# Performance work log

Hardware: AMD Instinct MI355X
Metric: run time of the kernel (lower is better)

## Reference

```python
import jax, jax.numpy as jnp
import numpy as np

NUM_HEADS = 16
HIDDEN = 1024
B, S = 2, 2048


def setup_inputs() -> dict:
    key = jax.random.key(0)
    ks = jax.random.split(key, 14)
    D = HIDDEN
    scale = 1.0 / np.sqrt(D)
    inp = {
        "query": jax.random.normal(ks[0], (B, S, D), jnp.float32),
        "key_in": jax.random.normal(ks[1], (B, S, D), jnp.float32),
        "value": jax.random.normal(ks[2], (B, S, D), jnp.float32),
        "group_prob": jax.random.uniform(ks[3], (B, S, S), jnp.float32),
        "mask": jax.random.randint(ks[4], (B, S, S), 0, 2, jnp.int32),
        "wq_k": jax.random.normal(ks[5], (D, D), jnp.float32) * scale,
        "wq_b": jnp.zeros((D,), jnp.float32),
        "wk_k": jax.random.normal(ks[6], (D, D), jnp.float32) * scale,
        "wk_b": jnp.zeros((D,), jnp.float32),
        "wv_k": jax.random.normal(ks[7], (D, D), jnp.float32) * scale,
        "wv_b": jnp.zeros((D,), jnp.float32),
        "wo_k": jax.random.normal(ks[8], (D, D), jnp.float32) * scale,
        "wo_b": jnp.zeros((D,), jnp.float32),
    }
    return inp


def _split_heads(x, H):
    b, s, d = x.shape
    return x.reshape(b, s, H, d // H).transpose(0, 2, 1, 3)  # (B,H,S,dh)


def reference(query, key_in, value, group_prob, mask,
              wq_k, wq_b, wk_k, wk_b, wv_k, wv_b, wo_k, wo_b):
    H = NUM_HEADS
    dh = query.shape[-1] // H
    q = _split_heads(query @ wq_k + wq_b, H)
    k = _split_heads(key_in @ wk_k + wk_b, H)
    v = _split_heads(value @ wv_k + wv_b, H)
    # scaled dot-product logits (B,H,Sq,Sk)
    logits = jnp.einsum('bhqd,bhkd->bhqk', q, k) / jnp.sqrt(jnp.asarray(dh, q.dtype))
    neg = (1.0 - mask.astype(q.dtype)) * -1e9
    logits = logits + neg[:, None, :, :]
    attn = jax.nn.softmax(logits, axis=-1)
    # Tree Transformer modulation: post-softmax elementwise scale by group_prob
    attn = attn * group_prob[:, None, :, :]
    out = jnp.einsum('bhqk,bhkd->bhqd', attn, v)
    out = out.transpose(0, 2, 1, 3).reshape(query.shape[0], -1, H * dh)
    return out @ wo_k + wo_b
```

## Files before the change

kernel.cpp:

```cpp
#include <hip/hip_runtime.h>
#include <hip/hip_bf16.h>
#include <stdint.h>

#define B_ 2
#define S_ 2048
#define D_ 1024
#define H_ 16
#define DH 64

typedef __attribute__((ext_vector_type(4))) float f32x4;
typedef __attribute__((ext_vector_type(8))) short s16x8;
typedef __attribute__((ext_vector_type(4))) short s16x4;

__device__ inline short f2bf(float f) {
  union { float f; unsigned u; } v; v.f = f;
  unsigned r = (v.u + 0x7fffu + ((v.u >> 16) & 1u)) >> 16;
  return (short)r;
}

__device__ inline float bfbits_lo(unsigned u) {
  union { unsigned x; float f; } v; v.x = u << 16; return v.f;
}
__device__ inline float bfbits_hi(unsigned u) {
  union { unsigned x; float f; } v; v.x = u & 0xffff0000u; return v.f;
}

__device__ inline float exp2v(float x) {
  float r; asm("v_exp_f32 %0, %1" : "=v"(r) : "v"(x)); return r;
}
__device__ inline unsigned cvtpk(float a, float b) {
  unsigned r; asm("v_cvt_pk_bf16_f32 %0, %1, %2" : "=v"(r) : "v"(a), "v"(b));
  return r;
}

__global__ __launch_bounds__(256) void cvt3_f32_bf16(const float* __restrict__ a,
                                                     const float* __restrict__ b,
                                                     const float* __restrict__ c,
                                                     short* oa, short* ob, short* oc,
                                                     int n) {
  int z = blockIdx.y;
  const float* in = z == 0 ? a : (z == 1 ? b : c);
  short* out = z == 0 ? oa : (z == 1 ? ob : oc);
  int i = (blockIdx.x * 256 + threadIdx.x) * 4;
  if (i < n) {
    float4 v = *(const float4*)(in + i);
    s16x4 o;
    o.x = f2bf(v.x); o.y = f2bf(v.y); o.z = f2bf(v.z); o.w = f2bf(v.w);
    *(s16x4*)(out + i) = o;
  }
}

__global__ __launch_bounds__(256) void transpose_cvt4(
    const float* __restrict__ i0, const float* __restrict__ i1,
    const float* __restrict__ i2, const float* __restrict__ i3,
    short* o0, short* o1, short* o2, short* o3) {
  int z = blockIdx.z;
  const float* in = z == 0 ? i0 : (z == 1 ? i1 : (z == 2 ? i2 : i3));
  short* out = z == 0 ? o0 : (z == 1 ? o1 : (z == 2 ? o2 : o3));
  __shared__ float tile[32][33];
  int bx = blockIdx.x, by = blockIdx.y;
  int x = bx * 32 + threadIdx.x;
#pragma unroll
  for (int i = 0; i < 32; i += 8) {
    int y = by * 32 + threadIdx.y + i;
    tile[threadIdx.y + i][threadIdx.x] = in[(size_t)y * D_ + x];
  }
  __syncthreads();
  int ox = by * 32 + threadIdx.x;
#pragma unroll
  for (int i = 0; i < 32; i += 8) {
    int oy = bx * 32 + threadIdx.y + i;
    out[(size_t)oy * D_ + ox] = f2bf(tile[threadIdx.x][threadIdx.y + i]);
  }
}

__device__ inline void gload_lds16(const void* g, void* l) {
  __builtin_amdgcn_global_load_lds(
      (const __attribute__((address_space(1))) unsigned*)g,
      (__attribute__((address_space(3))) unsigned*)l, 16, 0, 0);
}

#define BM 128
#define BN 128
#define BK 32

__global__ __launch_bounds__(256) void gemm_bt3(
    const short* __restrict__ A0, const short* __restrict__ A1, const short* __restrict__ A2,
    const short* __restrict__ Bt0, const short* __restrict__ Bt1, const short* __restrict__ Bt2,
    const float* __restrict__ bs0, const float* __restrict__ bs1, const float* __restrict__ bs2,
    void* C0, void* C1, void* C2,
    short* __restrict__ vtout, int vtmode,
    const int* __restrict__ mask, const float* __restrict__ gp,
    short* __restrict__ mgpout, int nmg,
    int M, int N, int K, int f32out, float os0, float os1, float os2) {
  int z = blockIdx.y;
  if (z == 3) {
    int i = (blockIdx.x * 256 + threadIdx.x) * 4;
    int stride = gridDim.x * 256 * 4;
    for (; i < nmg; i += stride) {
      int4 m = *(const int4*)(mask + i);
      float4 g = *(const float4*)(gp + i);
      short b0 = f2bf(g.x); if (!b0) b0 = (short)0x0080;
      short b1 = f2bf(g.y); if (!b1) b1 = (short)0x0080;
      short b2 = f2bf(g.z); if (!b2) b2 = (short)0x0080;
      short b3 = f2bf(g.w); if (!b3) b3 = (short)0x0080;
      s16x4 o;
      o.x = m.x ? b0 : 0;
      o.y = m.y ? b1 : 0;
      o.z = m.z ? b2 : 0;
      o.w = m.w ? b3 : 0;
      *(s16x4*)(mgpout + i) = o;
    }
    return;
  }
  const short* A = z == 0 ? A0 : (z == 1 ? A1 : A2);
  const short* Bt = z == 0 ? Bt0 : (z == 1 ? Bt1 : Bt2);
  const float* bias = z == 0 ? bs0 : (z == 1 ? bs1 : bs2);
  void* C = z == 0 ? C0 : (z == 1 ? C1 : C2);
  float oscale = z == 0 ? os0 : (z == 1 ? os1 : os2);

  __shared__ __align__(16) short As[BM * BK];
  __shared__ __align__(16) short Bs[BN * BK];
  int tid = threadIdx.x;
  int lane = tid & 63, wave = tid >> 6;
  int l15 = lane & 15, l4 = lane >> 4;
  int ntn = N / BN;
  int bid = blockIdx.x;
  bid = ((bid & 7) << 5) | (bid >> 3);
  int bm = bid / ntn, bn = bid % ntn;
  int row0 = bm * BM, col0 = bn * BN;
  int wm = (wave >> 1) * 64, wn = (wave & 1) * 64;

  f32x4 acc[4][4] = {};

  for (int k0 = 0; k0 < K; k0 += BK) {
    __syncthreads();
#pragma unroll
    for (int it = 0; it < 2; ++it) {
      int ch = it * 256 + tid;
      int r = ch >> 2, c = (ch & 3) * 8;
      int ldsbase = (it * 256 + wave * 64) * 8;
      gload_lds16(A + (size_t)(row0 + r) * K + k0 + c, &As[ldsbase]);
      gload_lds16(Bt + (size_t)(col0 + r) * K + k0 + c, &Bs[ldsbase]);
    }
    __syncthreads();
    s16x8 af[4], bf[4];
#pragma unroll
    for (int mf = 0; mf < 4; ++mf)
      af[mf] = *(const s16x8*)&As[(wm + mf * 16 + l15) * BK + l4 * 8];
#pragma unroll
    for (int nf = 0; nf < 4; ++nf)
      bf[nf] = *(const s16x8*)&Bs[(wn + nf * 16 + l15) * BK + l4 * 8];
#pragma unroll
    for (int mf = 0; mf < 4; ++mf)
#pragma unroll
      for (int nf = 0; nf < 4; ++nf)
        acc[mf][nf] = __builtin_amdgcn_mfma_f32_16x16x32_bf16(af[mf], bf[nf],
                                                              acc[mf][nf], 0, 0, 0);
  }

  if (vtmode && z == 2) {
    int b = row0 >> 11;
    int h = (col0 + wn) >> 6;
    int sbase = (row0 & (S_ - 1)) + wm + l4 * 4;
    short* vtb = vtout + ((size_t)(b * H_ + h) * DH) * S_;
#pragma unroll
    for (int nf = 0; nf < 4; ++nf) {
      int dh = nf * 16 + l15;
      float bv = bias[col0 + wn + dh];
#pragma unroll
      for (int mf = 0; mf < 4; ++mf) {
        uint2 o;
        o.x = cvtpk(acc[mf][nf][0] + bv, acc[mf][nf][1] + bv);
        o.y = cvtpk(acc[mf][nf][2] + bv, acc[mf][nf][3] + bv);
        *(uint2*)&vtb[(size_t)dh * S_ + sbase + mf * 16] = o;
      }
    }
    return;
  }

#pragma unroll
  for (int nf = 0; nf < 4; ++nf) {
    int gcol = col0 + wn + nf * 16 + l15;
    float bv = bias[gcol];
#pragma unroll
    for (int mf = 0; mf < 4; ++mf) {
#pragma unroll
      for (int r = 0; r < 4; ++r) {
        int grow = row0 + wm + mf * 16 + l4 * 4 + r;
        float v = (acc[mf][nf][r] + bv) * oscale;
        if (f32out)
          ((float*)C)[(size_t)grow * N + gcol] = v;
        else
          ((short*)C)[(size_t)grow * N + gcol] = f2bf(v);
      }
    }
  }
}

#define QB 128
#define NB 64
#define NTILES (S_ / NB)
#define M0_SHIFT 12.0f

__global__ __launch_bounds__(256, 3) void attn_fused(const short* __restrict__ Qp,
                                                     const short* __restrict__ Kp,
                                                     const short* __restrict__ VT,
                                                     const short* __restrict__ MGP,
                                                     short* __restrict__ ctx) {
  __shared__ __align__(16) short Ks[2][64 * 64];
  __shared__ __align__(16) short Vs[2][64 * 64];
  __shared__ __align__(16) short Ps[4][32 * 64];

  int tid = threadIdx.x, lane = tid & 63, wave = tid >> 6;
  int l15 = lane & 15, l4 = lane >> 4;
  int q0 = blockIdx.x * QB;
  int bh = blockIdx.y;
  int b = bh >> 4, h = bh & 15;
  int wq = wave * 32;

  const short* Qbase = Qp + (size_t)b * S_ * D_ + (size_t)h * DH;
  const short* Kbase = Kp + (size_t)b * S_ * D_ + (size_t)h * DH;
  const short* Vbase = VT + (size_t)(b * H_ + h) * DH * S_;
  const short* Mrow0 = MGP + (size_t)b * S_ * S_ + (size_t)(q0 + wq + l15) * S_ + l4 * 4;
  const short* Mrow1 = Mrow0 + (size_t)16 * S_;

  int i0 = tid, i1 = 256 + tid;
  int r0 = i0 >> 3, c0 = (i0 & 7) ^ (r0 & 7);
  int r1 = i1 >> 3, c1 = (i1 & 7) ^ (r1 & 7);
  int ldsA = wave * 512;
  int ldsB = 2048 + wave * 512;

#define STAGE(kv0, buf)                                                       \
  do {                                                                        \
    gload_lds16(Kbase + (size_t)((kv0) + r0) * D_ + c0 * 8, &Ks[buf][ldsA]);  \
    gload_lds16(Kbase + (size_t)((kv0) + r1) * D_ + c1 * 8, &Ks[buf][ldsB]);  \
    gload_lds16(Vbase + (size_t)r0 * S_ + (kv0) + c0 * 8, &Vs[buf][ldsA]);    \
    gload_lds16(Vbase + (size_t)r1 * S_ + (kv0) + c1 * 8, &Vs[buf][ldsB]);    \
  } while (0)

  s16x8 qf[2][2];
#pragma unroll
  for (int mf = 0; mf < 2; ++mf)
#pragma unroll
    for (int ks = 0; ks < 2; ++ks)
      qf[mf][ks] = *(const s16x8*)(Qbase + (size_t)(q0 + wq + mf * 16 + l15) * D_ +
                                   ks * 32 + l4 * 8);

  float lsum[2] = {0.f, 0.f};
  f32x4 oacc[2][4] = {};

  STAGE(0, 0);

  int q7 = l15 & 7;
  short* Pw = &Ps[wave][0];
  int prow[2] = {l15 * 64, (16 + l15) * 64};

  for (int t = 0; t < NTILES; ++t) {
    int buf = t & 1;
    int kvt = t * NB;

    uint2 g2[2][4];
#pragma unroll
    for (int nf = 0; nf < 4; ++nf) {
      g2[0][nf] = *(const uint2*)(Mrow0 + kvt + nf * 16);
      g2[1][nf] = *(const uint2*)(Mrow1 + kvt + nf * 16);
    }
    __builtin_amdgcn_sched_barrier(0);
    if (t + 1 < NTILES) {
      STAGE((t + 1) * NB, buf ^ 1);
      __builtin_amdgcn_sched_barrier(0);
      asm volatile("s_waitcnt vmcnt(12)" ::: "memory");
    } else {
      __builtin_amdgcn_sched_barrier(0);
      asm volatile("s_waitcnt vmcnt(8)" ::: "memory");
    }
    __builtin_amdgcn_s_barrier();
    __builtin_amdgcn_sched_barrier(0);

    f32x4 sacc[2][4] = {};
    __builtin_amdgcn_s_setprio(1);
#pragma unroll
    for (int nf = 0; nf < 4; ++nf) {
      int R = nf * 16 + l15;
#pragma unroll
      for (int ks = 0; ks < 2; ++ks) {
        s16x8 kf = *(const s16x8*)&Ks[buf][R * 64 + (((ks * 4 + l4) ^ q7) * 8)];
#pragma unroll
        for (int mf = 0; mf < 2; ++mf)
          sacc[mf][nf] = __builtin_amdgcn_mfma_f32_16x16x32_bf16(kf, qf[mf][ks],
                                                                 sacc[mf][nf], 0, 0, 0);
      }
    }
    __builtin_amdgcn_s_setprio(0);

    float ee[2][4][4];
#pragma unroll
    for (int mf = 0; mf < 2; ++mf)
#pragma unroll
      for (int nf = 0; nf < 4; ++nf)
#pragma unroll
        for (int r = 0; r < 4; ++r)
          ee[mf][nf][r] = exp2v(sacc[mf][nf][r] - M0_SHIFT);

    if (t + 1 < NTILES)
      asm volatile("s_waitcnt vmcnt(4)" ::: "memory");
    else
      asm volatile("s_waitcnt vmcnt(0)" ::: "memory");
    __builtin_amdgcn_sched_barrier(0);

#pragma unroll
    for (int mf = 0; mf < 2; ++mf) {
#pragma unroll
      for (int nf = 0; nf < 4; ++nf) {
        float gv0 = bfbits_lo(g2[mf][nf].x), gv1 = bfbits_hi(g2[mf][nf].x);
        float gv2 = bfbits_lo(g2[mf][nf].y), gv3 = bfbits_hi(g2[mf][nf].y);
        float e0 = ee[mf][nf][0], e1 = ee[mf][nf][1];
        float e2 = ee[mf][nf][2], e3 = ee[mf][nf][3];
        lsum[mf] += (gv0 != 0.f) ? e0 : 0.f;
        lsum[mf] += (gv1 != 0.f) ? e1 : 0.f;
        lsum[mf] += (gv2 != 0.f) ? e2 : 0.f;
        lsum[mf] += (gv3 != 0.f) ? e3 : 0.f;
        uint2 wp;
        wp.x = cvtpk(e0 * gv0, e1 * gv1);
        wp.y = cvtpk(e2 * gv2, e3 * gv3);
        int gr = ((nf * 2 + (l4 >> 1)) ^ q7) * 8 + (l4 & 1) * 4;
        *(uint2*)&Pw[prow[mf] + gr] = wp;
      }
    }

    __builtin_amdgcn_s_setprio(1);
#pragma unroll
    for (int ks = 0; ks < 2; ++ks) {
      s16x8 pa[2];
#pragma unroll
      for (int mf = 0; mf < 2; ++mf)
        pa[mf] = *(const s16x8*)&Pw[prow[mf] + (((ks * 4 + l4) ^ q7) * 8)];
#pragma unroll
      for (int df = 0; df < 4; ++df) {
        s16x8 vf = *(const s16x8*)&Vs[buf][(df * 16 + l15) * 64 +
                                           (((ks * 4 + l4) ^ q7) * 8)];
#pragma unroll
        for (int mf = 0; mf < 2; ++mf)
          oacc[mf][df] = __builtin_amdgcn_mfma_f32_16x16x32_bf16(vf, pa[mf],
                                                                 oacc[mf][df], 0, 0, 0);
      }
    }
    __builtin_amdgcn_s_setprio(0);

    asm volatile("s_waitcnt lgkmcnt(0)" ::: "memory");
    __builtin_amdgcn_s_barrier();
  }
#undef STAGE

#pragma unroll
  for (int mf = 0; mf < 2; ++mf) {
    float ls = lsum[mf];
    ls += __shfl_xor(ls, 16);
    ls += __shfl_xor(ls, 32);
    float inv = 1.f / ls;
    short* crow = ctx + ((size_t)(b * S_ + q0 + wq + mf * 16 + l15)) * D_ + h * DH;
#pragma unroll
    for (int df = 0; df < 4; ++df) {
      uint2 o;
      o.x = cvtpk(oacc[mf][df][0] * inv, oacc[mf][df][1] * inv);
      o.y = cvtpk(oacc[mf][df][2] * inv, oacc[mf][df][3] * inv);
      *(uint2*)(crow + df * 16 + l4 * 4) = o;
    }
  }
}

extern "C" void kernel_launch(void* const* d_in, const int* in_sizes, int n_in,
                              void* d_out, int out_size, void* d_ws, size_t ws_size,
                              hipStream_t stream) {
  const float* query = (const float*)d_in[0];
  const float* key_in = (const float*)d_in[1];
  const float* value = (const float*)d_in[2];
  const float* group_prob = (const float*)d_in[3];
  const int* mask = (const int*)d_in[4];
  const float* wq_k = (const float*)d_in[5];
  const float* wq_b = (const float*)d_in[6];
  const float* wk_k = (const float*)d_in[7];
  const float* wk_b = (const float*)d_in[8];
  const float* wv_k = (const float*)d_in[9];
  const float* wv_b = (const float*)d_in[10];
  const float* wo_k = (const float*)d_in[11];
  const float* wo_b = (const float*)d_in[12];
  float* out = (float*)d_out;

  short* ws = (short*)d_ws;
  const size_t NT = (size_t)B_ * S_ * D_;
  short* qbf = ws;
  short* kbf = qbf + NT;
  short* vbf = kbf + NT;
  short* wqt = vbf + NT;
  short* wkt = wqt + (size_t)D_ * D_;
  short* wvt = wkt + (size_t)D_ * D_;
  short* wot = wvt + (size_t)D_ * D_;
  short* qp = wot + (size_t)D_ * D_;
  short* kp = qp + NT;
  short* vt = kp + NT;
  short* ctx = vt + NT;
  short* mgp = ws;

  int nblk = (int)(NT / 4 / 256);
  cvt3_f32_bf16<<<dim3(nblk, 3), 256, 0, stream>>>(query, key_in, value,
                                                   qbf, kbf, vbf, (int)NT);

  dim3 tb(32, 8);
  transpose_cvt4<<<dim3(D_ / 32, D_ / 32, 4), tb, 0, stream>>>(
      wq_k, wk_k, wv_k, wo_k, wqt, wkt, wvt, wot);

  int M = B_ * S_;
  int gblocks = (M / BM) * (D_ / BN);
  int nmg = B_ * S_ * S_;
  const float QSCALE = 0.125f * 1.4426950408889634f;
  gemm_bt3<<<dim3(gblocks, 4), 256, 0, stream>>>(
      qbf, kbf, vbf, wqt, wkt, wvt, wq_b, wk_b, wv_b, qp, kp, nullptr,
      vt, 1, mask, group_prob, ctx + NT , nmg,
      M, D_, D_, 0, QSCALE, 1.0f, 1.0f);

  dim3 ag(S_ / QB, B_ * H_);
  attn_fused<<<ag, 256, 0, stream>>>(qp, kp, vt, ctx + NT, ctx);

  gemm_bt3<<<dim3(gblocks, 1), 256, 0, stream>>>(
      ctx, ctx, ctx, wot, wot, wot, wo_b, wo_b, wo_b, out, out, out,
      nullptr, 0, nullptr, nullptr, nullptr, 0,
      M, D_, D_, 1, 1.0f, 1.0f, 1.0f);
}
```

Before: 175.2 us.

## Split attention over the KV dimension into two partitions and combine partials

The attention kernel now splits the key/value sequence into two halves along a new grid dimension. Each half writes unnormalized bf16 numerators and row sums to workspace, and a new combine kernel adds them and normalizes. Because the softmax uses a fixed shift rather than a running max, the partials combine by plain addition. This doubles the grid (from 512 to 1024 blocks) to fill more compute units, at the cost of an extra kernel launch, extra global traffic for the partials, and bf16 rounding of the unnormalized numerators.

```diff
diff --git a/kernel.cpp b/kernel.cpp
--- a/kernel.cpp
+++ b/kernel.cpp
@@ -23,6 +23,11 @@
 }
 __device__ inline float bfbits_hi(unsigned u) {
   union { unsigned x; float f; } v; v.x = u & 0xffff0000u; return v.f;
+}
+
+__device__ inline float bf2f(unsigned short b) {
+  union { unsigned u; float f; } v; v.u = ((unsigned)b) << 16;
+  return v.f;
 }
 
 __device__ inline float exp2v(float x) {
@@ -200,14 +205,16 @@
 
 #define QB 128
 #define NB 64
-#define NTILES (S_ / NB)
+#define NSPLIT 2
+#define NT_SPLIT (S_ / NB / NSPLIT)
 #define M0_SHIFT 12.0f
 
-__global__ __launch_bounds__(256, 3) void attn_fused(const short* __restrict__ Qp,
+__global__ __launch_bounds__(256, 3) void attn_split(const short* __restrict__ Qp,
                                                      const short* __restrict__ Kp,
                                                      const short* __restrict__ VT,
                                                      const short* __restrict__ MGP,
-                                                     short* __restrict__ ctx) {
+                                                     short* __restrict__ nump,
+                                                     float* __restrict__ lsump) {
   __shared__ __align__(16) short Ks[2][64 * 64];
   __shared__ __align__(16) short Vs[2][64 * 64];
   __shared__ __align__(16) short Ps[4][32 * 64];
@@ -217,12 +224,15 @@
   int q0 = blockIdx.x * QB;
   int bh = blockIdx.y;
   int b = bh >> 4, h = bh & 15;
+  int split = blockIdx.z;
+  int kv_base = split * (S_ / NSPLIT);
   int wq = wave * 32;
 
   const short* Qbase = Qp + (size_t)b * S_ * D_ + (size_t)h * DH;
   const short* Kbase = Kp + (size_t)b * S_ * D_ + (size_t)h * DH;
   const short* Vbase = VT + (size_t)(b * H_ + h) * DH * S_;
-  const short* Mrow0 = MGP + (size_t)b * S_ * S_ + (size_t)(q0 + wq + l15) * S_ + l4 * 4;
+  const short* Mrow0 = MGP + (size_t)b * S_ * S_ + (size_t)(q0 + wq + l15) * S_ +
+                       kv_base + l4 * 4;
   const short* Mrow1 = Mrow0 + (size_t)16 * S_;
 
   int i0 = tid, i1 = 256 + tid;
@@ -250,13 +260,13 @@
   float lsum[2] = {0.f, 0.f};
   f32x4 oacc[2][4] = {};
 
-  STAGE(0, 0);
+  STAGE(kv_base, 0);
 
   int q7 = l15 & 7;
   short* Pw = &Ps[wave][0];
   int prow[2] = {l15 * 64, (16 + l15) * 64};
 
-  for (int t = 0; t < NTILES; ++t) {
+  for (int t = 0; t < NT_SPLIT; ++t) {
     int buf = t & 1;
     int kvt = t * NB;
 
@@ -267,8 +277,8 @@
       g2[1][nf] = *(const uint2*)(Mrow1 + kvt + nf * 16);
     }
     __builtin_amdgcn_sched_barrier(0);
-    if (t + 1 < NTILES) {
-      STAGE((t + 1) * NB, buf ^ 1);
+    if (t + 1 < NT_SPLIT) {
+      STAGE(kv_base + (t + 1) * NB, buf ^ 1);
       __builtin_amdgcn_sched_barrier(0);
       asm volatile("s_waitcnt vmcnt(12)" ::: "memory");
     } else {
@@ -303,7 +313,7 @@
         for (int r = 0; r < 4; ++r)
           ee[mf][nf][r] = exp2v(sacc[mf][nf][r] - M0_SHIFT);
 
-    if (t + 1 < NTILES)
+    if (t + 1 < NT_SPLIT)
       asm volatile("s_waitcnt vmcnt(4)" ::: "memory");
     else
       asm volatile("s_waitcnt vmcnt(0)" ::: "memory");
@@ -353,21 +363,55 @@
   }
 #undef STAGE
 
+  short* npart = nump + (size_t)split * B_ * S_ * D_;
+  float* lpart = lsump + (size_t)split * B_ * H_ * S_ +
+                 (size_t)(b * H_ + h) * S_;
 #pragma unroll
   for (int mf = 0; mf < 2; ++mf) {
     float ls = lsum[mf];
     ls += __shfl_xor(ls, 16);
     ls += __shfl_xor(ls, 32);
-    float inv = 1.f / ls;
-    short* crow = ctx + ((size_t)(b * S_ + q0 + wq + mf * 16 + l15)) * D_ + h * DH;
+    int qrow = q0 + wq + mf * 16 + l15;
+    if (l4 == 0) lpart[qrow] = ls;
+    short* crow = npart + ((size_t)(b * S_ + qrow)) * D_ + h * DH;
 #pragma unroll
     for (int df = 0; df < 4; ++df) {
       uint2 o;
-      o.x = cvtpk(oacc[mf][df][0] * inv, oacc[mf][df][1] * inv);
-      o.y = cvtpk(oacc[mf][df][2] * inv, oacc[mf][df][3] * inv);
+      o.x = cvtpk(oacc[mf][df][0], oacc[mf][df][1]);
+      o.y = cvtpk(oacc[mf][df][2], oacc[mf][df][3]);
       *(uint2*)(crow + df * 16 + l4 * 4) = o;
     }
   }
+}
+
+__global__ __launch_bounds__(256) void combine_o(const short* __restrict__ nump,
+                                                 const float* __restrict__ lsump,
+                                                 short* __restrict__ ctx) {
+  size_t i = ((size_t)blockIdx.x * 256 + threadIdx.x) * 8;
+  int dcol = (int)(i & (D_ - 1));
+  size_t row = i >> 10;
+  int h = dcol >> 6;
+  int b = (int)(row >> 11);
+  int q = (int)(row & (S_ - 1));
+  size_t lidx = (size_t)(b * H_ + h) * S_ + q;
+  float l1 = lsump[lidx];
+  float l2 = lsump[(size_t)B_ * H_ * S_ + lidx];
+  float inv = 1.f / (l1 + l2);
+  s16x8 n1 = *(const s16x8*)(nump + i);
+  s16x8 n2 = *(const s16x8*)(nump + (size_t)B_ * S_ * D_ + i);
+  uint2 o0, o1;
+  float v0 = (bf2f((unsigned short)n1[0]) + bf2f((unsigned short)n2[0])) * inv;
+  float v1 = (bf2f((unsigned short)n1[1]) + bf2f((unsigned short)n2[1])) * inv;
+  float v2 = (bf2f((unsigned short)n1[2]) + bf2f((unsigned short)n2[2])) * inv;
+  float v3 = (bf2f((unsigned short)n1[3]) + bf2f((unsigned short)n2[3])) * inv;
+  float v4 = (bf2f((unsigned short)n1[4]) + bf2f((unsigned short)n2[4])) * inv;
+  float v5 = (bf2f((unsigned short)n1[5]) + bf2f((unsigned short)n2[5])) * inv;
+  float v6 = (bf2f((unsigned short)n1[6]) + bf2f((unsigned short)n2[6])) * inv;
+  float v7 = (bf2f((unsigned short)n1[7]) + bf2f((unsigned short)n2[7])) * inv;
+  o0.x = cvtpk(v0, v1); o0.y = cvtpk(v2, v3);
+  o1.x = cvtpk(v4, v5); o1.y = cvtpk(v6, v7);
+  *(uint2*)(ctx + i) = o0;
+  *(uint2*)(ctx + i + 4) = o1;
 }
 
 extern "C" void kernel_launch(void* const* d_in, const int* in_sizes, int n_in,
@@ -401,7 +445,9 @@
   short* kp = qp + NT;
   short* vt = kp + NT;
   short* ctx = vt + NT;
-  short* mgp = ws;
+  short* mgp = ctx + NT;
+  short* nump = qbf;
+  float* lsump = (float*)vbf;
 
   int nblk = (int)(NT / 4 / 256);
   cvt3_f32_bf16<<<dim3(nblk, 3), 256, 0, stream>>>(query, key_in, value,
@@ -417,11 +463,13 @@
   const float QSCALE = 0.125f * 1.4426950408889634f;
   gemm_bt3<<<dim3(gblocks, 4), 256, 0, stream>>>(
       qbf, kbf, vbf, wqt, wkt, wvt, wq_b, wk_b, wv_b, qp, kp, nullptr,
-      vt, 1, mask, group_prob, ctx + NT , nmg,
+      vt, 1, mask, group_prob, mgp, nmg,
       M, D_, D_, 0, QSCALE, 1.0f, 1.0f);
 
-  dim3 ag(S_ / QB, B_ * H_);
-  attn_fused<<<ag, 256, 0, stream>>>(qp, kp, vt, ctx + NT, ctx);
+  dim3 ag(S_ / QB, B_ * H_, NSPLIT);
+  attn_split<<<ag, 256, 0, stream>>>(qp, kp, vt, mgp, nump, lsump);
+
+  combine_o<<<(int)(NT / 8 / 256), 256, 0, stream>>>(nump, lsump, ctx);
 
   gemm_bt3<<<dim3(gblocks, 1), 256, 0, stream>>>(
       ctx, ctx, ctx, wot, wot, wot, wo_b, wo_b, wo_b, out, out, out,
```

After: 191.9 us. 1.1x slower.
